# Optimization experiments

Hardware: AMD Instinct MI355X
Metric: run time of the kernel (lower is better)

The kernel has to match this reference:

```python
import jax, jax.numpy as jnp
import numpy as np

M0, M1, H = 128, 64, 8            # scalar mul, vector mul, num heads
AH0, AH1 = 16, 8                  # per-head irreps: 16x0e + 8x1e
D = M0 + 3 * M1                   # 320 node feature dim
DTP0 = M0 + M1                    # 192 scalar channels out of depthwise TP
DTP1 = M0 + 2 * M1                # 256 vector channels out of depthwise TP
WNUM = 2 * M0 + 3 * M1            # 448 TP path weights (uvu, edge mul=1)
RAD_IN, RAD_HID = 32, 64
N_NODES, N_EDGES = 10000, 160000
INV_SQRT3 = 1.0 / np.sqrt(3.0)    # CG norm for 1e x 1e -> 0e
INV_SQRT2 = 1.0 / np.sqrt(2.0)    # CG norm for 1e x 1e -> 1e


def _split(x, m0, m1):
    # e3nn layout: [m0 scalars | m1 vectors * 3 components]
    return x[..., :m0], x[..., m0:].reshape(x.shape[:-1] + (m1, 3))


def _silu(x):
    return x * jax.nn.sigmoid(x)


def _smooth_leaky(x, a=0.2):
    # SmoothLeakyReLU from equiformer
    return 0.5 * (1 + a) * x + 0.5 * (1 - a) * x * (2.0 * jax.nn.sigmoid(x) - 1.0)


def _dtp(s, v, e0, e1, w):
    # depthwise (uvu) tensor product of (M0x0e + M1x1e) with edge attr (1x0e + 1x1e)
    # s [E,M0], v [E,M1,3], e0 [E,1], e1 [E,3], w [E,WNUM] or [WNUM] (internal)
    w1, w2, w3, w4, w5 = jnp.split(w, [M0, 2 * M0, 2 * M0 + M1, 2 * M0 + 2 * M1], axis=-1)
    os1 = w1 * s * e0                                                  # 0e x 0e -> 0e
    os2 = w4 * (jnp.einsum('emc,ec->em', v, e1) * INV_SQRT3)           # 1e x 1e -> 0e
    ov1 = (w2 * s)[..., None] * e1[:, None, :]                         # 0e x 1e -> 1e
    ov2 = w3[..., None] * v * e0[..., None]                            # 1e x 0e -> 1e
    ov3 = w5[..., None] * (jnp.cross(v, e1[:, None, :]) * INV_SQRT2)   # 1e x 1e -> 1e
    return jnp.concatenate([os1, os2], -1), jnp.concatenate([ov1, ov2, ov3], -2)


def _forward(node_input, edge_src, edge_dst, edge_attr, edge_scalars,
             Wsrc_s, Wsrc_v, bsrc, Wdst_s, Wdst_v,
             rad_W1, rad_b1, rad_W2, rad_off,
             Wact_s, bact, Wact_v, Walpha, balpha, w_int,
             Wval_s, bval, Wval_v, alpha_dot, Wproj_s, bproj, Wproj_v):
    N = node_input.shape[0]
    E = edge_src.shape[0]
    s, v = _split(node_input, M0, M1)
    # merge_src / merge_dst: per-irrep linear (bias only on scalars of src)
    ms_s = s @ Wsrc_s + bsrc
    ms_v = jnp.einsum('nmc,mk->nkc', v, Wsrc_v)
    md_s = s @ Wdst_s
    md_v = jnp.einsum('nmc,mk->nkc', v, Wdst_v)
    msg_s = ms_s[edge_src] + md_s[edge_dst]          # [E, M0]
    msg_v = ms_v[edge_src] + md_v[edge_dst]          # [E, M1, 3]
    e0, e1 = edge_attr[:, :1], edge_attr[:, 1:4]
    # radial profile MLP -> edge-dependent TP weights
    w = _silu(edge_scalars @ rad_W1 + rad_b1) @ rad_W2 + rad_off       # [E, WNUM]
    ds, dv = _dtp(msg_s, msg_v, e0, e1, w)           # [E, DTP0], [E, DTP1, 3]
    # alpha branch: linear on TP scalars -> heads -> smooth leaky -> dot
    al = _smooth_leaky((ds @ Walpha + balpha).reshape(E, H, AH0))
    logits = jnp.einsum('ehk,hk->eh', al, alpha_dot[0])                # [E, H]
    # value branch: sep_act.lin + gate
    scal = ds @ Wact_s + bact                        # [E, M0+M1] scalars+gates
    gated_v = jnp.einsum('emc,mk->ekc', dv, Wact_v)  # [E, M1, 3]
    val_s = _silu(scal[:, :M0])
    val_v = gated_v * jax.nn.sigmoid(scal[:, M0:])[..., None]
    # sep_value: depthwise TP with internal weights + linear
    vs, vv = _dtp(val_s, val_v, e0, e1, w_int)
    out_s = vs @ Wval_s + bval                       # [E, H*AH0]
    out_v = jnp.einsum('emc,mk->ekc', vv, Wval_v)    # [E, H*AH1, 3]
    value = jnp.concatenate([out_s.reshape(E, H, AH0),
                             out_v.reshape(E, H, AH1 * 3)], axis=2)    # [E, H, 40]
    # softmax over incoming edges per destination node
    mx = jax.lax.stop_gradient(jax.ops.segment_max(logits, edge_dst, num_segments=N))
    mx = jnp.where(jnp.isfinite(mx), mx, 0.0)
    ex = jnp.exp(logits - mx[edge_dst])
    den = jax.ops.segment_sum(ex, edge_dst, num_segments=N)
    alpha = ex / (den[edge_dst] + 1e-16)             # [E, H]
    agg = jax.ops.segment_sum(value * alpha[..., None], edge_dst, num_segments=N)
    # heads2vec + output projection
    node_s = agg[:, :, :AH0].reshape(N, H * AH0)
    node_v = agg[:, :, AH0:].reshape(N, H * AH1, 3)
    po_s = node_s @ Wproj_s + bproj
    po_v = jnp.einsum('nmc,mk->nkc', node_v, Wproj_v)
    return jnp.concatenate([po_s, po_v.reshape(N, M1 * 3)], axis=1)


def _lin(key, fi, fo):
    return jax.random.normal(key, (fi, fo), jnp.float32) / np.sqrt(fi)


def setup_inputs() -> dict:
    ks = iter(jax.random.split(jax.random.key(0), 40))
    inp = {}
    inp['node_input'] = jax.random.normal(next(ks), (N_NODES, D), jnp.float32)
    inp['edge_src'] = jax.random.randint(next(ks), (N_EDGES,), 0, N_NODES)
    inp['edge_dst'] = jax.random.randint(next(ks), (N_EDGES,), 0, N_NODES)
    inp['edge_attr'] = jax.random.normal(next(ks), (N_EDGES, 4), jnp.float32)
    inp['edge_scalars'] = jax.random.normal(next(ks), (N_EDGES, RAD_IN), jnp.float32)
    inp['Wsrc_s'] = _lin(next(ks), M0, M0)
    inp['Wsrc_v'] = _lin(next(ks), M1, M1)
    inp['bsrc'] = 0.1 * jax.random.normal(next(ks), (M0,), jnp.float32)
    inp['Wdst_s'] = _lin(next(ks), M0, M0)
    inp['Wdst_v'] = _lin(next(ks), M1, M1)
    inp['rad_W1'] = _lin(next(ks), RAD_IN, RAD_HID)
    inp['rad_b1'] = 0.1 * jax.random.normal(next(ks), (RAD_HID,), jnp.float32)
    inp['rad_W2'] = _lin(next(ks), RAD_HID, WNUM)
    inp['rad_off'] = 0.1 * jax.random.normal(next(ks), (WNUM,), jnp.float32)
    inp['Wact_s'] = _lin(next(ks), DTP0, M0 + M1)
    inp['bact'] = 0.1 * jax.random.normal(next(ks), (M0 + M1,), jnp.float32)
    inp['Wact_v'] = _lin(next(ks), DTP1, M1)
    inp['Walpha'] = _lin(next(ks), DTP0, H * AH0)
    inp['balpha'] = 0.1 * jax.random.normal(next(ks), (H * AH0,), jnp.float32)
    inp['w_int'] = jax.random.normal(next(ks), (WNUM,), jnp.float32)
    inp['Wval_s'] = _lin(next(ks), DTP0, H * AH0)
    inp['bval'] = 0.1 * jax.random.normal(next(ks), (H * AH0,), jnp.float32)
    inp['Wval_v'] = _lin(next(ks), DTP1, H * AH1)
    inp['alpha_dot'] = jax.random.normal(next(ks), (1, H, AH0), jnp.float32) / np.sqrt(AH0)
    inp['Wproj_s'] = _lin(next(ks), H * AH0, M0)
    inp['bproj'] = 0.1 * jax.random.normal(next(ks), (M0,), jnp.float32)
    inp['Wproj_v'] = _lin(next(ks), H * AH1, M1)
    return inp


def reference(node_input, edge_src, edge_dst, edge_attr, edge_scalars,
              Wsrc_s, Wsrc_v, bsrc, Wdst_s, Wdst_v,
              rad_W1, rad_b1, rad_W2, rad_off,
              Wact_s, bact, Wact_v, Walpha, balpha, w_int,
              Wval_s, bval, Wval_v, alpha_dot, Wproj_s, bproj, Wproj_v):
    return _forward(node_input, edge_src, edge_dst, edge_attr, edge_scalars,
                    Wsrc_s, Wsrc_v, bsrc, Wdst_s, Wdst_v,
                    rad_W1, rad_b1, rad_W2, rad_off,
                    Wact_s, bact, Wact_v, Walpha, balpha, w_int,
                    Wval_s, bval, Wval_v, alpha_dot, Wproj_s, bproj, Wproj_v)
```

## Files before the change

kernel.cpp:

```cpp
#include <hip/hip_runtime.h>

#define NN 10000
#define NE 160000
#define INV_SQRT3f 0.57735026918962576f
#define INV_SQRT2f 0.70710678118654752f
#define VPL 640000

typedef short bshort8 __attribute__((ext_vector_type(8)));
typedef float floatx4 __attribute__((ext_vector_type(4)));
#define MFMA16(a,b,c) __builtin_amdgcn_mfma_f32_16x16x32_bf16((a),(b),(c),0,0,0)

__device__ __forceinline__ float sigm(float x){ return 1.f/(1.f+__expf(-x)); }
__device__ __forceinline__ float siluf(float x){ return x*sigm(x); }
__device__ __forceinline__ float sleaky(float x){ return 0.6f*x + 0.4f*x*(2.f*sigm(x)-1.f); }
__device__ __forceinline__ unsigned short f2bf(float f){
  return (unsigned short)((__float_as_uint(f) + 0x8000u)>>16);
}
__device__ __forceinline__ float bf2f(unsigned short h){
  return __uint_as_float(((unsigned)h)<<16);
}

#define O_W1   0
#define O_W2   2048
#define O_WAS  30720
#define O_WAVT 67584
#define O_WAVB 75776
#define O_WVS  83968
#define O_WVVT 108544
#define O_WVVB 116736
#define O_WALP 124928
#define SWZ_TOTAL 149504

__global__ __launch_bounds__(256) void k_init(float* __restrict__ num,
                                              float* __restrict__ den,
                                              int* __restrict__ cnt) {
  int i = blockIdx.x*256 + threadIdx.x;
  if (i < NN*320) num[i] = 0.f;
  if (i < NN*8) den[i] = 0.f;
  if (i < NN) cnt[i] = 0;
}

__global__ __launch_bounds__(256) void k_hist(const int* __restrict__ edst,
                                              int* __restrict__ cnt) {
  int e = blockIdx.x*256 + threadIdx.x;
  if (e < NE) atomicAdd(&cnt[edst[e]], 1);
}

__global__ __launch_bounds__(256) void k_scan(const int* __restrict__ cnt,
                                              int* __restrict__ offs) {
  __shared__ int wsum[4];
  const int tid = threadIdx.x;
  const int lane = tid & 63, wave = tid >> 6;
  int v[40]; int s = 0;
  #pragma unroll
  for (int j=0;j<40;j++){ int i = tid*40+j; v[j] = (i<NN)?cnt[i]:0; s += v[j]; }
  int incl = s;
  #pragma unroll
  for (int d=1; d<64; d<<=1) { int t = __shfl_up(incl, d, 64); if (lane>=d) incl += t; }
  if (lane==63) wsum[wave] = incl;
  __syncthreads();
  int wbase = 0;
  for (int w=0; w<wave; ++w) wbase += wsum[w];
  int excl = wbase + incl - s;
  #pragma unroll
  for (int j=0;j<40;j++){ int i = tid*40+j; if (i<NN) offs[i] = excl; excl += v[j]; }
}

__global__ __launch_bounds__(256) void k_scatter(const int* __restrict__ edst,
                                                 int* __restrict__ offs,
                                                 int* __restrict__ perm) {
  int e = blockIdx.x*256 + threadIdx.x;
  if (e < NE) {
    int pos = atomicAdd(&offs[edst[e]], 1);
    perm[pos] = e;
  }
}

__global__ __launch_bounds__(256) void node_pre(
    const float* __restrict__ x,
    const float* __restrict__ Wsrc_s, const float* __restrict__ Wsrc_v,
    const float* __restrict__ bsrc,
    const float* __restrict__ Wdst_s, const float* __restrict__ Wdst_v,
    float* __restrict__ ms_s, float* __restrict__ md_s,
    float* __restrict__ ms_v, float* __restrict__ md_v) {
  __shared__ __align__(16) float s_s[128*8];
  __shared__ __align__(16) float s_v[192*8];
  const int tid = threadIdx.x;
  const int n0 = blockIdx.x*8;
  for (int idx = tid; idx < 8*320; idx += 256) {
    int n = idx/320, d = idx - n*320;
    float val = x[(n0+n)*320 + d];
    if (d < 128) s_s[d*8+n] = val;
    else         s_v[(d-128)*8+n] = val;
  }
  __syncthreads();
  {
    int g = tid>>7, j = tid&127;
    float accs[4], accd[4];
    float b = bsrc[j];
    #pragma unroll
    for (int i=0;i<4;i++){ accs[i]=b; accd[i]=0.f; }
    for (int k=0;k<128;k++) {
      float w1 = Wsrc_s[k*128+j], w2 = Wdst_s[k*128+j];
      float4 sv = *(const float4*)&s_s[k*8+g*4];
      accs[0]+=sv.x*w1; accs[1]+=sv.y*w1; accs[2]+=sv.z*w1; accs[3]+=sv.w*w1;
      accd[0]+=sv.x*w2; accd[1]+=sv.y*w2; accd[2]+=sv.z*w2; accd[3]+=sv.w*w2;
    }
    #pragma unroll
    for (int i=0;i<4;i++){ int n=n0+g*4+i; ms_s[n*128+j]=accs[i]; md_s[n*128+j]=accd[i]; }
  }
  if (tid < 192) {
    int c = tid>>6, k = tid&63;
    float accs[8], accd[8];
    #pragma unroll
    for (int e=0;e<8;e++){ accs[e]=0.f; accd[e]=0.f; }
    for (int m=0;m<64;m++) {
      float w1 = Wsrc_v[m*64+k], w2 = Wdst_v[m*64+k];
      float4 v0 = *(const float4*)&s_v[(m*3+c)*8];
      float4 v1 = *(const float4*)&s_v[(m*3+c)*8+4];
      accs[0]+=v0.x*w1; accs[1]+=v0.y*w1; accs[2]+=v0.z*w1; accs[3]+=v0.w*w1;
      accs[4]+=v1.x*w1; accs[5]+=v1.y*w1; accs[6]+=v1.z*w1; accs[7]+=v1.w*w1;
      accd[0]+=v0.x*w2; accd[1]+=v0.y*w2; accd[2]+=v0.z*w2; accd[3]+=v0.w*w2;
      accd[4]+=v1.x*w2; accd[5]+=v1.y*w2; accd[6]+=v1.z*w2; accd[7]+=v1.w*w2;
    }
    #pragma unroll
    for (int e=0;e<8;e++){
      int n=n0+e;
      ms_v[c*VPL + n*64 + k] = accs[e];
      md_v[c*VPL + n*64 + k] = accd[e];
    }
  }
}

__global__ __launch_bounds__(256) void k_prep(
    const float* __restrict__ W1, const float* __restrict__ W2,
    const float* __restrict__ WAs, const float* __restrict__ WAv,
    const float* __restrict__ WVs, const float* __restrict__ WVv,
    const float* __restrict__ WAl,
    unsigned short* __restrict__ swz) {
  int s = blockIdx.x*256 + threadIdx.x;
  if (s >= SWZ_TOTAL) return;
  const float* src; int base, N, KT, rowOff;
  if      (s < 2048)  { base=O_W1;   src=W1;  N=64;  KT=1; rowOff=0; }
  else if (s < 30720) { base=O_W2;   src=W2;  N=448; KT=2; rowOff=0; }
  else if (s < 67584) { base=O_WAS;  src=WAs; N=192; KT=6; rowOff=0; }
  else if (s < 75776) { base=O_WAVT; src=WAv; N=64;  KT=4; rowOff=0; }
  else if (s < 83968) { base=O_WAVB; src=WAv; N=64;  KT=4; rowOff=128; }
  else if (s < 108544){ base=O_WVS;  src=WVs; N=128; KT=6; rowOff=0; }
  else if (s < 116736){ base=O_WVVT; src=WVv; N=64;  KT=4; rowOff=0; }
  else if (s < 124928){ base=O_WVVB; src=WVv; N=64;  KT=4; rowOff=128; }
  else                { base=O_WALP; src=WAl; N=128; KT=6; rowOff=0; }
  int loc = s - base;
  int j = loc & 7, l = (loc>>3)&63, kt = (loc>>9)%KT, nt = loc/(512*KT);
  int row = kt*32 + (l>>4)*8 + j + rowOff;
  int col = nt*16 + (l&15);
  swz[s] = f2bf(src[row*N + col]);
}

__global__ __launch_bounds__(256, 4) void e_all(
    const float* __restrict__ ms_s, const float* __restrict__ md_s,
    const float* __restrict__ ms_v, const float* __restrict__ md_v,
    const int* __restrict__ esrc, const int* __restrict__ edst,
    const int* __restrict__ perm,
    const float* __restrict__ eattr, const float* __restrict__ escal,
    const float* __restrict__ rad_b1, const float* __restrict__ rad_off,
    const float* __restrict__ bact, const float* __restrict__ w_int,
    const float* __restrict__ bval,
    const float* __restrict__ balpha, const float* __restrict__ alpha_dot,
    const unsigned short* __restrict__ swz,
    float* __restrict__ den, float* __restrict__ num) {
  __shared__ __align__(16) char smem[39040];
  unsigned short* sw   = (unsigned short*)smem;
  float* vout          = (float*)smem;
  unsigned short* ads  = (unsigned short*)(smem+14336);
  unsigned short* at1  = (unsigned short*)(smem+20736);
  unsigned short* advb = (unsigned short*)(smem+25088);
  unsigned short* aes  = (unsigned short*)(smem+25088);
  unsigned short* ah   = (unsigned short*)(smem+26368);
  float* s_e0 = (float*)(smem+38144);
  float* s_e1 = (float*)(smem+38208);
  float* s_ex = (float*)(smem+38400);
  int* s_src  = (int*)(smem+38912);
  int* s_dst  = (int*)(smem+38976);
  int* s_eid  = (int*)(smem+38848);
  const int tid  = threadIdx.x;
  const int lane = tid & 63, wave = tid >> 6;
  const int quad = lane >> 4, l15 = lane & 15;
  const int eb = blockIdx.x*16;

  if (tid < 16) {
    int eid = perm[eb+tid];
    s_eid[tid] = eid; s_src[tid] = esrc[eid]; s_dst[tid] = edst[eid];
  }
  __syncthreads();
  if (tid >= 64 && tid < 128) {
    int t = tid-64, e = t>>2, q = t&3;
    float a = eattr[s_eid[e]*4+q];
    if (q == 0) s_e0[e] = a; else s_e1[(q-1)*16+e] = a;
  }
  #pragma unroll
  for (int it = 0; it < 2; ++it) {
    int idx = tid + it*256;
    int e = idx>>5, i = idx&31;
    aes[e*40+i] = f2bf(escal[s_eid[e]*32+i]);
  }
  __syncthreads();

  {
    int nt = wave, col = nt*16 + l15;
    bshort8 a = *(const bshort8*)&aes[l15*40 + quad*8];
    bshort8 b = *(const bshort8*)&swz[O_W1 + (nt*64 + lane)*8];
    float bb = rad_b1[col];
    floatx4 acc = {bb,bb,bb,bb};
    acc = MFMA16(a, b, acc);
    #pragma unroll
    for (int r=0;r<4;r++) ah[(quad*4+r)*72 + col] = f2bf(siluf(acc[r]));
  }
  __syncthreads();

  {
    bshort8 ha0 = *(const bshort8*)&ah[l15*72 + quad*8];
    bshort8 ha1 = *(const bshort8*)&ah[l15*72 + 32 + quad*8];
    #pragma unroll
    for (int t=0;t<7;t++) {
      int nt = wave*7 + t, col = nt*16 + l15;
      float o = rad_off[col];
      floatx4 acc = {o,o,o,o};
      acc = MFMA16(ha0, *(const bshort8*)&swz[O_W2 + ((nt*2+0)*64+lane)*8], acc);
      acc = MFMA16(ha1, *(const bshort8*)&swz[O_W2 + ((nt*2+1)*64+lane)*8], acc);
      #pragma unroll
      for (int r=0;r<4;r++) sw[(quad*4+r)*448 + col] = f2bf(acc[r]);
    }
  }
  __syncthreads();

  #pragma unroll
  for (int it = 0; it < 8; ++it) {
    int t = tid + it*256;
    int m = t&127, e = t>>7;
    float msgs = ms_s[s_src[e]*128+m] + md_s[s_dst[e]*128+m];
    ads[e*200+m] = f2bf(bf2f(sw[e*448+m])*msgs*s_e0[e]);
    at1[e*136+m] = f2bf(bf2f(sw[e*448+128+m])*msgs);
  }
  #pragma unroll
  for (int it = 0; it < 4; ++it) {
    int t = tid + it*256;
    int k = t&63, e = t>>6;
    int sb = s_src[e]*64 + k, db = s_dst[e]*64 + k;
    float vx = ms_v[0*VPL+sb] + md_v[0*VPL+db];
    float vy = ms_v[1*VPL+sb] + md_v[1*VPL+db];
    float vz = ms_v[2*VPL+sb] + md_v[2*VPL+db];
    float ex1 = s_e1[0+e], ey1 = s_e1[16+e], ez1 = s_e1[32+e];
    float d = vx*ex1 + vy*ey1 + vz*ez1;
    ads[e*200+128+k] = f2bf(bf2f(sw[e*448+320+k])*d*INV_SQRT3f);
    float w3v = bf2f(sw[e*448+256+k])*s_e0[e];
    float w5  = bf2f(sw[e*448+384+k])*INV_SQRT2f;
    advb[0*2176 + e*136 + k] = f2bf(w3v*vx);
    advb[1*2176 + e*136 + k] = f2bf(w3v*vy);
    advb[2*2176 + e*136 + k] = f2bf(w3v*vz);
    advb[0*2176 + e*136 + 64+k] = f2bf(w5*(vy*ez1 - vz*ey1));
    advb[1*2176 + e*136 + 64+k] = f2bf(w5*(vz*ex1 - vx*ez1));
    advb[2*2176 + e*136 + 64+k] = f2bf(w5*(vx*ey1 - vy*ex1));
  }
  __syncthreads();

  floatx4 sc0, sc1, sc2, gsa, gb0, gb1, gb2;
  {
    bshort8 fa[6];
    #pragma unroll
    for (int kt=0;kt<6;kt++) fa[kt] = *(const bshort8*)&ads[l15*200 + kt*32 + quad*8];
    #pragma unroll
    for (int t=0;t<2;t++) {
      int h = wave*2 + t;
      int col = h*16 + l15;
      float bb = balpha[col];
      floatx4 acc = {bb,bb,bb,bb};
      #pragma unroll
      for (int kt=0;kt<6;kt++)
        acc = MFMA16(fa[kt], *(const bshort8*)&swz[O_WALP + ((h*6+kt)*64+lane)*8], acc);
      float ad = alpha_dot[col];
      #pragma unroll
      for (int r=0;r<4;r++) {
        float p = sleaky(acc[r])*ad;
        p += __shfl_xor(p, 1);
        p += __shfl_xor(p, 2);
        p += __shfl_xor(p, 4);
        p += __shfl_xor(p, 8);
        if (l15 == 0) {
          int row = quad*4 + r;
          float ex = __expf(p);
          s_ex[row*8+h] = ex;
          atomicAdd(&den[s_dst[row]*8+h], ex);
        }
      }
    }
    {
      float bb = bact[wave*16 + l15];
      floatx4 a0 = {bb,bb,bb,bb};
      #pragma unroll
      for (int kt=0;kt<6;kt++)
        a0 = MFMA16(fa[kt], *(const bshort8*)&swz[O_WAS + ((wave*6+kt)*64+lane)*8], a0);
      sc0 = a0;
    }
    {
      float bb = bact[(wave+4)*16 + l15];
      floatx4 a1 = {bb,bb,bb,bb};
      #pragma unroll
      for (int kt=0;kt<6;kt++)
        a1 = MFMA16(fa[kt], *(const bshort8*)&swz[O_WAS + (((wave+4)*6+kt)*64+lane)*8], a1);
      sc1 = a1;
    }
    {
      float bb = bact[(wave+8)*16 + l15];
      floatx4 a2 = {bb,bb,bb,bb};
      #pragma unroll
      for (int kt=0;kt<6;kt++)
        a2 = MFMA16(fa[kt], *(const bshort8*)&swz[O_WAS + (((wave+8)*6+kt)*64+lane)*8], a2);
      sc2 = a2;
    }
    bshort8 ft[4];
    #pragma unroll
    for (int kt=0;kt<4;kt++) ft[kt] = *(const bshort8*)&at1[l15*136 + kt*32 + quad*8];
    {
      floatx4 acc = {0.f,0.f,0.f,0.f};
      #pragma unroll
      for (int kt=0;kt<4;kt++)
        acc = MFMA16(ft[kt], *(const bshort8*)&swz[O_WAVT + ((wave*4+kt)*64+lane)*8], acc);
      gsa = acc;
    }
    #pragma unroll
    for (int c=0;c<3;c++) {
      floatx4 acc = {0.f,0.f,0.f,0.f};
      #pragma unroll
      for (int kt=0;kt<4;kt++) {
        bshort8 fb = *(const bshort8*)&advb[c*2176 + l15*136 + kt*32 + quad*8];
        acc = MFMA16(fb, *(const bshort8*)&swz[O_WAVB + ((wave*4+kt)*64+lane)*8], acc);
      }
      if (c==0) gb0 = acc; else if (c==1) gb1 = acc; else gb2 = acc;
    }
  }
  __syncthreads();

  {
    const int k = wave*16 + l15;
    #pragma unroll
    for (int r=0;r<4;r++) {
      int row = quad*4 + r;
      float e0 = s_e0[row];
      {
        float v = siluf(sc0[r]);
        ads[row*200+k] = f2bf(w_int[k]*v*e0);
        at1[row*136+k] = f2bf(w_int[128+k]*v);
      }
      {
        int m = 64+k;
        float v = siluf(sc1[r]);
        ads[row*200+m] = f2bf(w_int[m]*v*e0);
        at1[row*136+m] = f2bf(w_int[128+m]*v);
      }
      {
        float sg = sigm(sc2[r]);
        float gs = gsa[r];
        float ex1 = s_e1[0+row], ey1 = s_e1[16+row], ez1 = s_e1[32+row];
        float v0 = (gs*ex1 + gb0[r])*sg;
        float v1 = (gs*ey1 + gb1[r])*sg;
        float v2 = (gs*ez1 + gb2[r])*sg;
        float d = v0*ex1 + v1*ey1 + v2*ez1;
        ads[row*200+128+k] = f2bf(w_int[320+k]*d*INV_SQRT3f);
        float w3v = w_int[256+k]*e0;
        float w5  = w_int[384+k]*INV_SQRT2f;
        advb[0*2176 + row*136 + k] = f2bf(w3v*v0);
        advb[1*2176 + row*136 + k] = f2bf(w3v*v1);
        advb[2*2176 + row*136 + k] = f2bf(w3v*v2);
        advb[0*2176 + row*136 + 64+k] = f2bf(w5*(v1*ez1 - v2*ey1));
        advb[1*2176 + row*136 + 64+k] = f2bf(w5*(v2*ex1 - v0*ez1));
        advb[2*2176 + row*136 + 64+k] = f2bf(w5*(v0*ey1 - v1*ex1));
      }
    }
  }
  __syncthreads();

  {
    bshort8 fa[6];
    #pragma unroll
    for (int kt=0;kt<6;kt++) fa[kt] = *(const bshort8*)&ads[l15*200 + kt*32 + quad*8];
    #pragma unroll
    for (int t=0;t<2;t++) {
      int h = wave + 4*t;
      float bb = bval[h*16 + l15];
      floatx4 acc = {bb,bb,bb,bb};
      #pragma unroll
      for (int kt=0;kt<6;kt++)
        acc = MFMA16(fa[kt], *(const bshort8*)&swz[O_WVS + ((h*6+kt)*64+lane)*8], acc);
      #pragma unroll
      for (int r=0;r<4;r++) {
        int row = quad*4 + r;
        vout[row*128 + h*16 + l15] = acc[r]*s_ex[row*8+h];
      }
    }
  }
  __syncthreads();

  {
    int j = tid & 127, g = tid >> 7;
    int h = j>>4, jj = j&15;
    float acc = 0.f; int cur = s_dst[g*8];
    #pragma unroll
    for (int e = g*8; e < g*8+8; ++e) {
      int d = s_dst[e];
      if (d != cur) { atomicAdd(&num[cur*320 + h*40 + jj], acc); acc = 0.f; cur = d; }
      acc += vout[e*128 + j];
    }
    atomicAdd(&num[cur*320 + h*40 + jj], acc);
  }
  __syncthreads();

  {
    bshort8 ft[4];
    #pragma unroll
    for (int kt=0;kt<4;kt++) ft[kt] = *(const bshort8*)&at1[l15*136 + kt*32 + quad*8];
    floatx4 vsh = {0.f,0.f,0.f,0.f};
    #pragma unroll
    for (int kt=0;kt<4;kt++)
      vsh = MFMA16(ft[kt], *(const bshort8*)&swz[O_WVVT + ((wave*4+kt)*64+lane)*8], vsh);
    int k = wave*16 + l15;
    int h = k>>3, q = k&7;
    #pragma unroll
    for (int c=0;c<3;c++) {
      floatx4 acc = {0.f,0.f,0.f,0.f};
      #pragma unroll
      for (int kt=0;kt<4;kt++) {
        bshort8 fb = *(const bshort8*)&advb[c*2176 + l15*136 + kt*32 + quad*8];
        acc = MFMA16(fb, *(const bshort8*)&swz[O_WVVB + ((wave*4+kt)*64+lane)*8], acc);
      }
      #pragma unroll
      for (int r=0;r<4;r++) {
        int row = quad*4 + r;
        vout[row*192 + h*24 + q*3 + c] =
            (acc[r] + s_e1[c*16+row]*vsh[r]) * s_ex[row*8+h];
      }
    }
  }
  __syncthreads();

  #pragma unroll
  for (int it = 0; it < 2; ++it) {
    int idx = tid + it*256;
    if (idx < 384) {
      int g = idx/192, jj = idx - g*192;
      int h = jj/24, rr = jj - h*24;
      float acc = 0.f; int cur = s_dst[g*8];
      #pragma unroll
      for (int e = g*8; e < g*8+8; ++e) {
        int d = s_dst[e];
        if (d != cur) { atomicAdd(&num[cur*320 + h*40 + 16 + rr], acc); acc = 0.f; cur = d; }
        acc += vout[e*192 + jj];
      }
      atomicAdd(&num[cur*320 + h*40 + 16 + rr], acc);
    }
  }
}

__global__ __launch_bounds__(256) void node_post(
    const float* __restrict__ num, const float* __restrict__ den,
    const float* __restrict__ Wproj_s, const float* __restrict__ bproj,
    const float* __restrict__ Wproj_v, float* __restrict__ out) {
  __shared__ __align__(16) float s_ns[128*8];
  __shared__ __align__(16) float s_nv[192*8];
  const int tid = threadIdx.x;
  const int n0 = blockIdx.x*8;
  for (int idx = tid; idx < 8*320; idx += 256) {
    int n = idx/320, j = idx - n*320;
    int h = j/40, r = j - h*40;
    float a = num[(n0+n)*320+j] / (den[(n0+n)*8+h] + 1e-16f);
    if (r < 16) s_ns[(h*16+r)*8+n] = a;
    else        s_nv[(h*24 + (r-16))*8+n] = a;
  }
  __syncthreads();
  {
    int g = tid>>7, j = tid&127;
    float acc[4]; float b = bproj[j];
    #pragma unroll
    for (int i=0;i<4;i++) acc[i]=b;
    for (int k=0;k<128;k++) {
      float wv = Wproj_s[k*128+j];
      float4 s4 = *(const float4*)&s_ns[k*8+g*4];
      acc[0]+=s4.x*wv; acc[1]+=s4.y*wv; acc[2]+=s4.z*wv; acc[3]+=s4.w*wv;
    }
    #pragma unroll
    for (int i=0;i<4;i++) out[(n0+g*4+i)*320 + j] = acc[i];
  }
  if (tid < 192) {
    int c = tid>>6, k = tid&63;
    float acc[8];
    #pragma unroll
    for (int e=0;e<8;e++) acc[e]=0.f;
    for (int m=0;m<64;m++) {
      float wv = Wproj_v[m*64+k];
      float4 v0 = *(const float4*)&s_nv[(m*3+c)*8];
      float4 v1 = *(const float4*)&s_nv[(m*3+c)*8+4];
      acc[0]+=v0.x*wv; acc[1]+=v0.y*wv; acc[2]+=v0.z*wv; acc[3]+=v0.w*wv;
      acc[4]+=v1.x*wv; acc[5]+=v1.y*wv; acc[6]+=v1.z*wv; acc[7]+=v1.w*wv;
    }
    #pragma unroll
    for (int e=0;e<8;e++) out[(n0+e)*320 + 128 + k*3 + c] = acc[e];
  }
}

extern "C" void kernel_launch(void* const* d_in, const int* in_sizes, int n_in,
                              void* d_out, int out_size, void* d_ws, size_t ws_size,
                              hipStream_t stream) {
  (void)in_sizes; (void)n_in; (void)out_size; (void)ws_size;
  const float* node_input = (const float*)d_in[0];
  const int*   esrc       = (const int*)d_in[1];
  const int*   edst       = (const int*)d_in[2];
  const float* eattr      = (const float*)d_in[3];
  const float* escal      = (const float*)d_in[4];
  const float* Wsrc_s     = (const float*)d_in[5];
  const float* Wsrc_v     = (const float*)d_in[6];
  const float* bsrc       = (const float*)d_in[7];
  const float* Wdst_s     = (const float*)d_in[8];
  const float* Wdst_v     = (const float*)d_in[9];
  const float* rad_W1     = (const float*)d_in[10];
  const float* rad_b1     = (const float*)d_in[11];
  const float* rad_W2     = (const float*)d_in[12];
  const float* rad_off    = (const float*)d_in[13];
  const float* Wact_s     = (const float*)d_in[14];
  const float* bact       = (const float*)d_in[15];
  const float* Wact_v     = (const float*)d_in[16];
  const float* Walpha     = (const float*)d_in[17];
  const float* balpha     = (const float*)d_in[18];
  const float* w_int      = (const float*)d_in[19];
  const float* Wval_s     = (const float*)d_in[20];
  const float* bval       = (const float*)d_in[21];
  const float* Wval_v     = (const float*)d_in[22];
  const float* alpha_dot  = (const float*)d_in[23];
  const float* Wproj_s    = (const float*)d_in[24];
  const float* bproj      = (const float*)d_in[25];
  const float* Wproj_v    = (const float*)d_in[26];
  float* out = (float*)d_out;

  float* ws = (float*)d_ws;
  float* ms_s   = ws;
  float* md_s   = ws + 1280000;
  float* ms_v   = ws + 2560000;
  float* md_v   = ws + 4480000;
  float* den    = ws + 6400000;
  float* num    = ws + 6480000;
  unsigned short* swz = (unsigned short*)(ws + 9680000);
  int* cnt  = (int*)(ws + 9754752);
  int* offs = (int*)(ws + 9764752);
  int* perm = (int*)(ws + 9774752);

  k_prep<<<584, 256, 0, stream>>>(rad_W1, rad_W2, Wact_s, Wact_v, Wval_s, Wval_v, Walpha, swz);
  k_init<<<12500, 256, 0, stream>>>(num, den, cnt);
  k_hist<<<625, 256, 0, stream>>>(edst, cnt);
  k_scan<<<1, 256, 0, stream>>>(cnt, offs);
  k_scatter<<<625, 256, 0, stream>>>(edst, offs, perm);
  node_pre<<<1250, 256, 0, stream>>>(node_input, Wsrc_s, Wsrc_v, bsrc, Wdst_s, Wdst_v,
                                     ms_s, md_s, ms_v, md_v);
  e_all<<<10000, 256, 0, stream>>>(ms_s, md_s, ms_v, md_v, esrc, edst, perm, eattr, escal,
                                   rad_b1, rad_off, bact, w_int, bval,
                                   balpha, alpha_dot, swz, den, num);
  node_post<<<1250, 256, 0, stream>>>(num, den, Wproj_s, bproj, Wproj_v, out);
}
```

Baseline: 448.4 us.

## Fuse radial weight epilogue into TP scalars and scatter directly from MFMA registers

The radial MLP second layer now computes the scalar-path weights and immediately multiplies them by the gathered messages in registers, so only the vector-path weights are staged in shared memory. The value and vector-output scatters now do run-length accumulation straight from the MFMA accumulators over each quad's 4 rows, dropping the vout staging buffers and two barriers. Shared memory shrinks, which allows raising the launch bound to 5 blocks per SM. Block indices are also swizzled to spread sorted edges across XCDs. The trade-off is more atomics per destination, since runs are now 4 rows instead of 8, plus higher register pressure under the tighter bound.

Result: slower. 499.9 us (+11.5%).

```diff
diff --git a/kernel.cpp b/kernel.cpp
--- a/kernel.cpp
+++ b/kernel.cpp
@@ -157,7 +157,7 @@
   swz[s] = f2bf(src[row*N + col]);
 }
 
-__global__ __launch_bounds__(256, 4) void e_all(
+__global__ __launch_bounds__(256, 5) void e_all(
     const float* __restrict__ ms_s, const float* __restrict__ md_s,
     const float* __restrict__ ms_v, const float* __restrict__ md_v,
     const int* __restrict__ esrc, const int* __restrict__ edst,
@@ -169,24 +169,24 @@
     const float* __restrict__ balpha, const float* __restrict__ alpha_dot,
     const unsigned short* __restrict__ swz,
     float* __restrict__ den, float* __restrict__ num) {
-  __shared__ __align__(16) char smem[39040];
-  unsigned short* sw   = (unsigned short*)smem;
-  float* vout          = (float*)smem;
-  unsigned short* ads  = (unsigned short*)(smem+14336);
-  unsigned short* at1  = (unsigned short*)(smem+20736);
-  unsigned short* advb = (unsigned short*)(smem+25088);
-  unsigned short* aes  = (unsigned short*)(smem+25088);
-  unsigned short* ah   = (unsigned short*)(smem+26368);
-  float* s_e0 = (float*)(smem+38144);
-  float* s_e1 = (float*)(smem+38208);
-  float* s_ex = (float*)(smem+38400);
-  int* s_src  = (int*)(smem+38912);
-  int* s_dst  = (int*)(smem+38976);
-  int* s_eid  = (int*)(smem+38848);
+  __shared__ __align__(16) char smem[30912];
+  unsigned short* sw_v = (unsigned short*)smem;
+  unsigned short* ads  = (unsigned short*)(smem+6144);
+  unsigned short* at1  = (unsigned short*)(smem+12544);
+  unsigned short* advb = (unsigned short*)(smem+16896);
+  unsigned short* aes  = (unsigned short*)(smem+16896);
+  unsigned short* ah   = (unsigned short*)(smem+19456);
+  float* s_e0 = (float*)(smem+29952);
+  float* s_e1 = (float*)(smem+30016);
+  float* s_ex = (float*)(smem+30208);
+  int* s_eid  = (int*)(smem+30720);
+  int* s_src  = (int*)(smem+30784);
+  int* s_dst  = (int*)(smem+30848);
   const int tid  = threadIdx.x;
   const int lane = tid & 63, wave = tid >> 6;
   const int quad = lane >> 4, l15 = lane & 15;
-  const int eb = blockIdx.x*16;
+  const int bswz = (blockIdx.x & 7)*1250 + (blockIdx.x >> 3);
+  const int eb = bswz*16;
 
   if (tid < 16) {
     int eid = perm[eb+tid];
@@ -221,27 +221,40 @@
   {
     bshort8 ha0 = *(const bshort8*)&ah[l15*72 + quad*8];
     bshort8 ha1 = *(const bshort8*)&ah[l15*72 + 32 + quad*8];
-    #pragma unroll
-    for (int t=0;t<7;t++) {
-      int nt = wave*7 + t, col = nt*16 + l15;
+    int src_[4], dst_[4];
+    #pragma unroll
+    for (int r=0;r<4;r++){ int e=quad*4+r; src_[r]=s_src[e]; dst_[r]=s_dst[e]; }
+    #pragma unroll
+    for (int p=0;p<2;p++) {
+      int nt1 = wave*2+p, nt2 = nt1+8;
+      int m = nt1*16 + l15;
+      float o1 = rad_off[m], o2 = rad_off[128+m];
+      floatx4 a1 = {o1,o1,o1,o1}, a2 = {o2,o2,o2,o2};
+      a1 = MFMA16(ha0, *(const bshort8*)&swz[O_W2 + ((nt1*2+0)*64+lane)*8], a1);
+      a1 = MFMA16(ha1, *(const bshort8*)&swz[O_W2 + ((nt1*2+1)*64+lane)*8], a1);
+      a2 = MFMA16(ha0, *(const bshort8*)&swz[O_W2 + ((nt2*2+0)*64+lane)*8], a2);
+      a2 = MFMA16(ha1, *(const bshort8*)&swz[O_W2 + ((nt2*2+1)*64+lane)*8], a2);
+      #pragma unroll
+      for (int r=0;r<4;r++) {
+        int e = quad*4+r;
+        float msgs = ms_s[src_[r]*128+m] + md_s[dst_[r]*128+m];
+        ads[e*200+m] = f2bf(a1[r]*msgs*s_e0[e]);
+        at1[e*136+m] = f2bf(a2[r]*msgs);
+      }
+    }
+    #pragma unroll
+    for (int q=0;q<3;q++) {
+      int nt = 16 + wave*3 + q, col = nt*16 + l15;
       float o = rad_off[col];
       floatx4 acc = {o,o,o,o};
       acc = MFMA16(ha0, *(const bshort8*)&swz[O_W2 + ((nt*2+0)*64+lane)*8], acc);
       acc = MFMA16(ha1, *(const bshort8*)&swz[O_W2 + ((nt*2+1)*64+lane)*8], acc);
       #pragma unroll
-      for (int r=0;r<4;r++) sw[(quad*4+r)*448 + col] = f2bf(acc[r]);
-    }
-  }
-  __syncthreads();
-
-  #pragma unroll
-  for (int it = 0; it < 8; ++it) {
-    int t = tid + it*256;
-    int m = t&127, e = t>>7;
-    float msgs = ms_s[s_src[e]*128+m] + md_s[s_dst[e]*128+m];
-    ads[e*200+m] = f2bf(bf2f(sw[e*448+m])*msgs*s_e0[e]);
-    at1[e*136+m] = f2bf(bf2f(sw[e*448+128+m])*msgs);
-  }
+      for (int r=0;r<4;r++) sw_v[(quad*4+r)*192 + (col-256)] = f2bf(acc[r]);
+    }
+  }
+  __syncthreads();
+
   #pragma unroll
   for (int it = 0; it < 4; ++it) {
     int t = tid + it*256;
@@ -252,9 +265,9 @@
     float vz = ms_v[2*VPL+sb] + md_v[2*VPL+db];
     float ex1 = s_e1[0+e], ey1 = s_e1[16+e], ez1 = s_e1[32+e];
     float d = vx*ex1 + vy*ey1 + vz*ez1;
-    ads[e*200+128+k] = f2bf(bf2f(sw[e*448+320+k])*d*INV_SQRT3f);
-    float w3v = bf2f(sw[e*448+256+k])*s_e0[e];
-    float w5  = bf2f(sw[e*448+384+k])*INV_SQRT2f;
+    ads[e*200+128+k] = f2bf(bf2f(sw_v[e*192+64+k])*d*INV_SQRT3f);
+    float w3v = bf2f(sw_v[e*192+k])*s_e0[e];
+    float w5  = bf2f(sw_v[e*192+128+k])*INV_SQRT2f;
     advb[0*2176 + e*136 + k] = f2bf(w3v*vx);
     advb[1*2176 + e*136 + k] = f2bf(w3v*vy);
     advb[2*2176 + e*136 + k] = f2bf(w3v*vz);
@@ -279,6 +292,7 @@
       for (int kt=0;kt<6;kt++)
         acc = MFMA16(fa[kt], *(const bshort8*)&swz[O_WALP + ((h*6+kt)*64+lane)*8], acc);
       float ad = alpha_dot[col];
+      float exv[4];
       #pragma unroll
       for (int r=0;r<4;r++) {
         float p = sleaky(acc[r])*ad;
@@ -286,12 +300,19 @@
         p += __shfl_xor(p, 2);
         p += __shfl_xor(p, 4);
         p += __shfl_xor(p, 8);
-        if (l15 == 0) {
-          int row = quad*4 + r;
-          float ex = __expf(p);
-          s_ex[row*8+h] = ex;
-          atomicAdd(&den[s_dst[row]*8+h], ex);
+        float ex = __expf(p);
+        exv[r] = ex;
+        if (l15 == 0) s_ex[(quad*4+r)*8+h] = ex;
+      }
+      if (l15 == 0) {
+        float racc = exv[0]; int cur = s_dst[quad*4];
+        #pragma unroll
+        for (int r=1;r<4;r++) {
+          int d = s_dst[quad*4+r];
+          if (d != cur) { atomicAdd(&den[cur*8+h], racc); racc = 0.f; cur = d; }
+          racc += exv[r];
         }
+        atomicAdd(&den[cur*8+h], racc);
       }
     }
     {
@@ -392,29 +413,18 @@
       #pragma unroll
       for (int kt=0;kt<6;kt++)
         acc = MFMA16(fa[kt], *(const bshort8*)&swz[O_WVS + ((h*6+kt)*64+lane)*8], acc);
-      #pragma unroll
-      for (int r=0;r<4;r++) {
-        int row = quad*4 + r;
-        vout[row*128 + h*16 + l15] = acc[r]*s_ex[row*8+h];
-      }
-    }
-  }
-  __syncthreads();
-
-  {
-    int j = tid & 127, g = tid >> 7;
-    int h = j>>4, jj = j&15;
-    float acc = 0.f; int cur = s_dst[g*8];
-    #pragma unroll
-    for (int e = g*8; e < g*8+8; ++e) {
-      int d = s_dst[e];
-      if (d != cur) { atomicAdd(&num[cur*320 + h*40 + jj], acc); acc = 0.f; cur = d; }
-      acc += vout[e*128 + j];
-    }
-    atomicAdd(&num[cur*320 + h*40 + jj], acc);
-  }
-  __syncthreads();
-
+      float racc = acc[0]*s_ex[(quad*4+0)*8+h];
+      int cur = s_dst[quad*4];
+      #pragma unroll
+      for (int r=1;r<4;r++) {
+        int d = s_dst[quad*4+r];
+        float val = acc[r]*s_ex[(quad*4+r)*8+h];
+        if (d != cur) { atomicAdd(&num[cur*320 + h*40 + l15], racc); racc = 0.f; cur = d; }
+        racc += val;
+      }
+      atomicAdd(&num[cur*320 + h*40 + l15], racc);
+    }
+  }
   {
     bshort8 ft[4];
     #pragma unroll
@@ -423,8 +433,9 @@
     #pragma unroll
     for (int kt=0;kt<4;kt++)
       vsh = MFMA16(ft[kt], *(const bshort8*)&swz[O_WVVT + ((wave*4+kt)*64+lane)*8], vsh);
-    int k = wave*16 + l15;
-    int h = k>>3, q = k&7;
+    const int k = wave*16 + l15;
+    const int h = k>>3, q = k&7;
+    floatx4 vb0, vb1, vb2;
     #pragma unroll
     for (int c=0;c<3;c++) {
       floatx4 acc = {0.f,0.f,0.f,0.f};
@@ -433,31 +444,29 @@
         bshort8 fb = *(const bshort8*)&advb[c*2176 + l15*136 + kt*32 + quad*8];
         acc = MFMA16(fb, *(const bshort8*)&swz[O_WVVB + ((wave*4+kt)*64+lane)*8], acc);
       }
-      #pragma unroll
-      for (int r=0;r<4;r++) {
-        int row = quad*4 + r;
-        vout[row*192 + h*24 + q*3 + c] =
-            (acc[r] + s_e1[c*16+row]*vsh[r]) * s_ex[row*8+h];
-      }
-    }
-  }
-  __syncthreads();
-
-  #pragma unroll
-  for (int it = 0; it < 2; ++it) {
-    int idx = tid + it*256;
-    if (idx < 384) {
-      int g = idx/192, jj = idx - g*192;
-      int h = jj/24, rr = jj - h*24;
-      float acc = 0.f; int cur = s_dst[g*8];
-      #pragma unroll
-      for (int e = g*8; e < g*8+8; ++e) {
-        int d = s_dst[e];
-        if (d != cur) { atomicAdd(&num[cur*320 + h*40 + 16 + rr], acc); acc = 0.f; cur = d; }
-        acc += vout[e*192 + jj];
-      }
-      atomicAdd(&num[cur*320 + h*40 + 16 + rr], acc);
-    }
+      if (c==0) vb0 = acc; else if (c==1) vb1 = acc; else vb2 = acc;
+    }
+    float a0 = 0.f, a1 = 0.f, a2 = 0.f;
+    int cur = s_dst[quad*4];
+    float* base = &num[0];
+    #pragma unroll
+    for (int r=0;r<4;r++) {
+      int row = quad*4 + r;
+      int d = s_dst[row];
+      if (d != cur) {
+        atomicAdd(&base[cur*320 + h*40 + 16 + q*3 + 0], a0);
+        atomicAdd(&base[cur*320 + h*40 + 16 + q*3 + 1], a1);
+        atomicAdd(&base[cur*320 + h*40 + 16 + q*3 + 2], a2);
+        a0 = a1 = a2 = 0.f; cur = d;
+      }
+      float ex = s_ex[row*8+h];
+      a0 += (vb0[r] + s_e1[0*16+row]*vsh[r])*ex;
+      a1 += (vb1[r] + s_e1[1*16+row]*vsh[r])*ex;
+      a2 += (vb2[r] + s_e1[2*16+row]*vsh[r])*ex;
+    }
+    atomicAdd(&base[cur*320 + h*40 + 16 + q*3 + 0], a0);
+    atomicAdd(&base[cur*320 + h*40 + 16 + q*3 + 1], a1);
+    atomicAdd(&base[cur*320 + h*40 + 16 + q*3 + 2], a2);
   }
 }
 
```
